# Kernel optimization log

Measured on AMD Instinct MI355X. Metric: run time of the kernel, lower is better.

Reference implementation:

```python
import jax, jax.numpy as jnp
import numpy as np

B, D, O, E, K = 8192, 2048, 2048, 8, 2


def setup_inputs() -> dict:
    key = jax.random.key(0)
    k1, k2, k3, k4 = jax.random.split(key, 4)
    x = jax.random.normal(k1, (B, D), dtype=jnp.float32)
    # router: Linear(D -> E)
    router_w = jax.random.normal(k2, (E, D), dtype=jnp.float32) * (1.0 / np.sqrt(D))
    router_b = jnp.zeros((E,), dtype=jnp.float32)
    # experts: [E, O, D] weight (xavier-uniform-like scale), [E, O] bias (zeros)
    lim = np.sqrt(6.0 / (D + O))
    expert_w = jax.random.uniform(k3, (E, O, D), dtype=jnp.float32, minval=-lim, maxval=lim)
    expert_b = jnp.zeros((E, O), dtype=jnp.float32)
    return {"x": x, "router_w": router_w, "router_b": router_b,
            "expert_w": expert_w, "expert_b": expert_b}


def reference(x, router_w, router_b, expert_w, expert_b):
    # router logits [B, E]
    logits = x @ router_w.T + router_b
    top_vals, top_idx = jax.lax.top_k(logits, K)          # [B, K]
    routing_weights = jax.nn.softmax(top_vals, axis=-1)   # softmax over top-k logits
    # dense per-(token, expert) combine weight [B, E]; zero for unselected experts
    onehot = jax.nn.one_hot(top_idx, E, dtype=x.dtype)    # [B, K, E]
    w_be = jnp.einsum('bk,bke->be', routing_weights, onehot)
    # per-expert linear, weighted combine (loop over small fixed E)
    out = jnp.zeros((x.shape[0], O), dtype=x.dtype)
    for e in range(E):
        out = out + w_be[:, e:e + 1] * (x @ expert_w[e].T + expert_b[e])
    return out
```

## Files before the change

### kernel.cpp

```cpp
#include <hip/hip_runtime.h>
#include <stdint.h>

#define NB 8192
#define ND 2048
#define NO 2048
#define NE 8
#define NT (ND / 32)

typedef __bf16 bf16x8 __attribute__((ext_vector_type(8)));
typedef float floatx4 __attribute__((ext_vector_type(4)));

__device__ __forceinline__ unsigned short f2bf(float f) {
    union { float f; uint32_t u; } v; v.f = f;
    uint32_t u = v.u;
    return (unsigned short)((u + 0x7FFFu + ((u >> 16) & 1u)) >> 16);
}

__global__ __launch_bounds__(256) void cvt_bf16_kernel(
        const float* __restrict__ b, unsigned short* __restrict__ ob, int n4) {
    int i = blockIdx.x * blockDim.x + threadIdx.x;
    int stride = gridDim.x * blockDim.x;
    for (; i < n4; i += stride) {
        float4 v = ((const float4*)b)[i];
        ushort4 o;
        o.x = f2bf(v.x); o.y = f2bf(v.y); o.z = f2bf(v.z); o.w = f2bf(v.w);
        ((ushort4*)ob)[i] = o;
    }
}

__global__ __launch_bounds__(256) void router_topk_kernel(const float* __restrict__ x,
        const float* __restrict__ rw, const float* __restrict__ rb,
        unsigned short* __restrict__ xbf,
        int* __restrict__ i0a, int* __restrict__ i1a,
        float* __restrict__ w0a, float* __restrict__ w1a) {
    const int wave = threadIdx.x >> 6;
    const int lane = threadIdx.x & 63;
    const int t = blockIdx.x * 4 + wave;
    const float4* xp = (const float4*)(x + (size_t)t * ND);
    const float4* rp = (const float4*)rw;
    ushort4* xo = (ushort4*)(xbf + (size_t)t * ND);
    float acc[NE];
#pragma unroll
    for (int e = 0; e < NE; e++) acc[e] = 0.f;
#pragma unroll
    for (int i = 0; i < ND / 256; i++) {
        int idx = i * 64 + lane;
        float4 xv = xp[idx];
        ushort4 o;
        o.x = f2bf(xv.x); o.y = f2bf(xv.y); o.z = f2bf(xv.z); o.w = f2bf(xv.w);
        xo[idx] = o;
#pragma unroll
        for (int e = 0; e < NE; e++) {
            float4 rv = rp[(size_t)e * (ND / 4) + idx];
            acc[e] += xv.x * rv.x + xv.y * rv.y + xv.z * rv.z + xv.w * rv.w;
        }
    }
#pragma unroll
    for (int e = 0; e < NE; e++) {
        float v = acc[e];
#pragma unroll
        for (int s = 32; s > 0; s >>= 1) v += __shfl_xor(v, s, 64);
        acc[e] = v;
    }
    if (lane == 0) {
        float lg[NE];
#pragma unroll
        for (int e = 0; e < NE; e++) lg[e] = acc[e] + rb[e];
        int i0 = 0; float v0 = lg[0];
#pragma unroll
        for (int e = 1; e < NE; e++) if (lg[e] > v0) { v0 = lg[e]; i0 = e; }
        int i1 = -1; float v1 = -3.4e38f;
#pragma unroll
        for (int e = 0; e < NE; e++) if (e != i0 && lg[e] > v1) { v1 = lg[e]; i1 = e; }
        float ex = expf(v1 - v0);
        float inv = 1.f / (1.f + ex);
        i0a[t] = i0; i1a[t] = i1;
        w0a[t] = inv; w1a[t] = ex * inv;
    }
}

__global__ __launch_bounds__(256) void compact_kernel(
        const int* __restrict__ i0a, const int* __restrict__ i1a,
        const float* __restrict__ w0a, const float* __restrict__ w1a,
        int* __restrict__ cnt, int* __restrict__ tok, float* __restrict__ wl) {
    const int lane = threadIdx.x & 63;
    const int gw = (blockIdx.x * 256 + threadIdx.x) >> 6;
    const int t = gw * 64 + lane;
#pragma unroll
    for (int which = 0; which < 2; which++) {
        int sel   = which ? i1a[t] : i0a[t];
        float w   = which ? w1a[t] : w0a[t];
        unsigned long long m[NE];
#pragma unroll
        for (int e = 0; e < NE; e++) m[e] = __ballot(sel == e);
        int slot = __popcll(m[sel] & ((1ull << lane) - 1ull));
        int base = 0;
        if (lane < NE) base = atomicAdd(&cnt[lane], (int)__popcll(m[lane]));
        base = __shfl(base, sel, 64);
        tok[sel * NB + base + slot] = t;
        wl[sel * NB + base + slot]  = w;
    }
}

#define GLL16(g, l) __builtin_amdgcn_global_load_lds( \
    (const __attribute__((address_space(1))) void*)(g), \
    (__attribute__((address_space(3))) void*)(l), 16, 0, 0)

__global__ __launch_bounds__(256, 3) void moe_gemm_kernel(
        const unsigned short* __restrict__ xbf, const unsigned short* __restrict__ wbf,
        const float* __restrict__ eb, const int* __restrict__ cntArr,
        const int* __restrict__ listTok, const float* __restrict__ listW,
        float* __restrict__ out) {
    __shared__ unsigned short sA[3][128 * 32];
    __shared__ unsigned short sB[3][128 * 32];
    __shared__ int sTok[128];
    __shared__ float sW[128];

    const int e = blockIdx.z, mt = blockIdx.y, nt = blockIdx.x;
    const int cnt = cntArr[e];
    if (mt * 128 >= cnt) return;
    const int tid = threadIdx.x;
    if (tid < 128) {
        int r = mt * 128 + tid;
        bool ok = r < cnt;
        sTok[tid] = ok ? listTok[e * NB + r] : 0;
        sW[tid]   = ok ? listW[e * NB + r] : 0.f;
    }
    __syncthreads();

    const char* gA[2]; const char* gB[2];
    int offAB[2];
#pragma unroll
    for (int r = 0; r < 2; r++) {
        int c = r * 256 + tid;
        int row = c >> 2, colb = (c & 3) * 16;
        gA[r] = (const char*)xbf + (size_t)sTok[row] * (ND * 2) + colb;
        gB[r] = (const char*)wbf + ((size_t)e * NO + (size_t)nt * 128 + row) * (ND * 2) + colb;
        offAB[r] = c * 16;
    }

    const int wave = tid >> 6, lane = tid & 63;
    const int wm = (wave >> 1) * 64, wn = (wave & 1) * 64;
    const int lr = lane & 15, lq = lane >> 4;
    int roA[4], roB[4];
#pragma unroll
    for (int i = 0; i < 4; i++) {
        roA[i] = (wm + i * 16 + lr) * 32 + lq * 8;
        roB[i] = (wn + i * 16 + lr) * 32 + lq * 8;
    }

    floatx4 acc[4][4];
#pragma unroll
    for (int mi = 0; mi < 4; mi++)
#pragma unroll
        for (int nj = 0; nj < 4; nj++) acc[mi][nj] = (floatx4){0.f, 0.f, 0.f, 0.f};

#pragma unroll
    for (int r = 0; r < 2; r++) {
        GLL16(gA[r], (char*)sA[0] + offAB[r]);
        GLL16(gB[r], (char*)sB[0] + offAB[r]);
        gA[r] += 64; gB[r] += 64;
    }
#pragma unroll
    for (int r = 0; r < 2; r++) {
        GLL16(gA[r], (char*)sA[1] + offAB[r]);
        GLL16(gB[r], (char*)sB[1] + offAB[r]);
        gA[r] += 64; gB[r] += 64;
    }

    int cur = 0;
#pragma unroll 1
    for (int t = 0; t < NT; t++) {
        int nxt = cur + 2; if (nxt >= 3) nxt -= 3;
        if (t + 2 < NT) {
#pragma unroll
            for (int r = 0; r < 2; r++) {
                GLL16(gA[r], (char*)sA[nxt] + offAB[r]);
                GLL16(gB[r], (char*)sB[nxt] + offAB[r]);
                gA[r] += 64; gB[r] += 64;
            }
            asm volatile("s_waitcnt vmcnt(8)" ::: "memory");
        } else if (t + 2 == NT) {
            asm volatile("s_waitcnt vmcnt(4)" ::: "memory");
        } else {
            asm volatile("s_waitcnt vmcnt(0)" ::: "memory");
        }
        __builtin_amdgcn_s_barrier();

        const unsigned short* sAc = sA[cur];
        const unsigned short* sBc = sB[cur];
        bf16x8 af[4], bfr[4];
#pragma unroll
        for (int mi = 0; mi < 4; mi++) af[mi] = *(const bf16x8*)&sAc[roA[mi]];
#pragma unroll
        for (int nj = 0; nj < 4; nj++) bfr[nj] = *(const bf16x8*)&sBc[roB[nj]];
#pragma unroll
        for (int mi = 0; mi < 4; mi++)
#pragma unroll
            for (int nj = 0; nj < 4; nj++)
                acc[mi][nj] = __builtin_amdgcn_mfma_f32_16x16x32_bf16(af[mi], bfr[nj], acc[mi][nj], 0, 0, 0);

        asm volatile("s_waitcnt lgkmcnt(0)" ::: "memory");
        __builtin_amdgcn_s_barrier();
        cur = cur + 1 == 3 ? 0 : cur + 1;
    }

#pragma unroll
    for (int nj = 0; nj < 4; nj++) {
        int gn = nt * 128 + wn + nj * 16 + lr;
        float bias = eb[(size_t)e * NO + gn];
#pragma unroll
        for (int mi = 0; mi < 4; mi++) {
#pragma unroll
            for (int r = 0; r < 4; r++) {
                int m = wm + mi * 16 + lq * 4 + r;
                if (mt * 128 + m < cnt) {
                    atomicAdd(out + (size_t)sTok[m] * NO + gn,
                              sW[m] * (acc[mi][nj][r] + bias));
                }
            }
        }
    }
}

extern "C" void kernel_launch(void* const* d_in, const int* in_sizes, int n_in,
                              void* d_out, int out_size, void* d_ws, size_t ws_size,
                              hipStream_t stream) {
    const float* x        = (const float*)d_in[0];
    const float* router_w = (const float*)d_in[1];
    const float* router_b = (const float*)d_in[2];
    const float* expert_w = (const float*)d_in[3];
    const float* expert_b = (const float*)d_in[4];
    float* out = (float*)d_out;
    char* ws = (char*)d_ws;

    unsigned short* xbf = (unsigned short*)ws;
    unsigned short* wbf = (unsigned short*)(ws + 33554432);
    size_t o = 100663296;
    int*   tokL = (int*)(ws + o);   o += NE * NB * 4;
    float* wL   = (float*)(ws + o); o += NE * NB * 4;
    int*   i0a  = (int*)(ws + o);   o += NB * 4;
    int*   i1a  = (int*)(ws + o);   o += NB * 4;
    float* w0a  = (float*)(ws + o); o += NB * 4;
    float* w1a  = (float*)(ws + o); o += NB * 4;
    int*   cnt  = (int*)(ws + o);   o += 128;

    hipMemsetAsync(cnt, 0, 128, stream);
    hipMemsetAsync(out, 0, (size_t)NB * NO * 4, stream);
    router_topk_kernel<<<NB / 4, 256, 0, stream>>>(x, router_w, router_b, xbf,
                                                   i0a, i1a, w0a, w1a);
    cvt_bf16_kernel<<<2048, 256, 0, stream>>>(expert_w, wbf, NE * NO * ND / 4);
    compact_kernel<<<NB / 64 / 4, 256, 0, stream>>>(i0a, i1a, w0a, w1a, cnt, tokL, wL);
    moe_gemm_kernel<<<dim3(NO / 128, NB / 128, NE), 256, 0, stream>>>(
        xbf, wbf, expert_b, cnt, tokL, wL, out);
}
```

Baseline: 591.4 us.

## Pre-gather routed token rows into packed per-expert bf16 buffer before GEMM

A new gather kernel converts x to bf16 and writes routed tokens contiguously per expert, so the MoE GEMM reads A rows sequentially instead of doing indirect per-row token loads. The output zeroing is folded into the weight-convert kernel and the counter reset moves into the router kernel, which removes two memsets. In exchange there is an extra pass that writes a 2*NB row buffer, and each GEMM block computes an expert prefix sum from the counts.

```diff
diff --git a/kernel.cpp b/kernel.cpp
--- a/kernel.cpp
+++ b/kernel.cpp
@@ -6,9 +6,12 @@
 #define NO 2048
 #define NE 8
 #define NT (ND / 32)
+#define NROWS (2 * NB)
+#define NROWS_PAD (NROWS + 128)
 
 typedef __bf16 bf16x8 __attribute__((ext_vector_type(8)));
 typedef float floatx4 __attribute__((ext_vector_type(4)));
+typedef unsigned short ushort8 __attribute__((ext_vector_type(8)));
 
 __device__ __forceinline__ unsigned short f2bf(float f) {
     union { float f; uint32_t u; } v; v.f = f;
@@ -16,29 +19,37 @@
     return (unsigned short)((u + 0x7FFFu + ((u >> 16) & 1u)) >> 16);
 }
 
-__global__ __launch_bounds__(256) void cvt_bf16_kernel(
-        const float* __restrict__ b, unsigned short* __restrict__ ob, int n4) {
+__global__ __launch_bounds__(256) void cvt_zero_kernel(
+        const float* __restrict__ w, unsigned short* __restrict__ ob,
+        float* __restrict__ out) {
+    const int n4W = NE * NO * ND / 4;
+    const int n4O = NB * NO / 4;
     int i = blockIdx.x * blockDim.x + threadIdx.x;
     int stride = gridDim.x * blockDim.x;
-    for (; i < n4; i += stride) {
-        float4 v = ((const float4*)b)[i];
-        ushort4 o;
-        o.x = f2bf(v.x); o.y = f2bf(v.y); o.z = f2bf(v.z); o.w = f2bf(v.w);
-        ((ushort4*)ob)[i] = o;
+    for (; i < n4W + n4O; i += stride) {
+        if (i < n4W) {
+            float4 v = ((const float4*)w)[i];
+            ushort4 o;
+            o.x = f2bf(v.x); o.y = f2bf(v.y); o.z = f2bf(v.z); o.w = f2bf(v.w);
+            ((ushort4*)ob)[i] = o;
+        } else {
+            float4 z = {0.f, 0.f, 0.f, 0.f};
+            ((float4*)out)[i - n4W] = z;
+        }
     }
 }
 
 __global__ __launch_bounds__(256) void router_topk_kernel(const float* __restrict__ x,
         const float* __restrict__ rw, const float* __restrict__ rb,
-        unsigned short* __restrict__ xbf,
         int* __restrict__ i0a, int* __restrict__ i1a,
-        float* __restrict__ w0a, float* __restrict__ w1a) {
+        float* __restrict__ w0a, float* __restrict__ w1a,
+        int* __restrict__ cnt) {
+    if (blockIdx.x == 0 && threadIdx.x < NE) cnt[threadIdx.x] = 0;
     const int wave = threadIdx.x >> 6;
     const int lane = threadIdx.x & 63;
     const int t = blockIdx.x * 4 + wave;
     const float4* xp = (const float4*)(x + (size_t)t * ND);
     const float4* rp = (const float4*)rw;
-    ushort4* xo = (ushort4*)(xbf + (size_t)t * ND);
     float acc[NE];
 #pragma unroll
     for (int e = 0; e < NE; e++) acc[e] = 0.f;
@@ -46,9 +57,6 @@
     for (int i = 0; i < ND / 256; i++) {
         int idx = i * 64 + lane;
         float4 xv = xp[idx];
-        ushort4 o;
-        o.x = f2bf(xv.x); o.y = f2bf(xv.y); o.z = f2bf(xv.z); o.w = f2bf(xv.w);
-        xo[idx] = o;
 #pragma unroll
         for (int e = 0; e < NE; e++) {
             float4 rv = rp[(size_t)e * (ND / 4) + idx];
@@ -102,12 +110,42 @@
     }
 }
 
+__global__ __launch_bounds__(256) void gather_kernel(
+        const float* __restrict__ x, const int* __restrict__ cnt,
+        const int* __restrict__ tokL, unsigned short* __restrict__ packed) {
+    int pre[NE + 1];
+    pre[0] = 0;
+#pragma unroll
+    for (int k = 0; k < NE; k++) pre[k + 1] = pre[k] + cnt[k];
+    const int CH = ND / 8;
+    int idx = blockIdx.x * blockDim.x + threadIdx.x;
+    const int stride = gridDim.x * blockDim.x;
+    const int tot = NROWS_PAD * CH;
+    for (; idx < tot; idx += stride) {
+        int p = idx >> 8;
+        int c = idx & (CH - 1);
+        int e = -1, r = 0;
+#pragma unroll
+        for (int k = 0; k < NE; k++)
+            if (p >= pre[k] && p < pre[k + 1]) { e = k; r = p - pre[k]; }
+        ushort8 o = (ushort8)0;
+        if (e >= 0) {
+            int tk = tokL[e * NB + r];
+            const float4* s = (const float4*)(x + (size_t)tk * ND + c * 8);
+            float4 a = s[0], b = s[1];
+            o[0] = f2bf(a.x); o[1] = f2bf(a.y); o[2] = f2bf(a.z); o[3] = f2bf(a.w);
+            o[4] = f2bf(b.x); o[5] = f2bf(b.y); o[6] = f2bf(b.z); o[7] = f2bf(b.w);
+        }
+        *(ushort8*)(packed + (size_t)p * ND + c * 8) = o;
+    }
+}
+
 #define GLL16(g, l) __builtin_amdgcn_global_load_lds( \
     (const __attribute__((address_space(1))) void*)(g), \
     (__attribute__((address_space(3))) void*)(l), 16, 0, 0)
 
 __global__ __launch_bounds__(256, 3) void moe_gemm_kernel(
-        const unsigned short* __restrict__ xbf, const unsigned short* __restrict__ wbf,
+        const unsigned short* __restrict__ packed, const unsigned short* __restrict__ wbf,
         const float* __restrict__ eb, const int* __restrict__ cntArr,
         const int* __restrict__ listTok, const float* __restrict__ listW,
         float* __restrict__ out) {
@@ -117,6 +155,8 @@
     __shared__ float sW[128];
 
     const int e = blockIdx.z, mt = blockIdx.y, nt = blockIdx.x;
+    int base = 0;
+    for (int i = 0; i < e; i++) base += cntArr[i];
     const int cnt = cntArr[e];
     if (mt * 128 >= cnt) return;
     const int tid = threadIdx.x;
@@ -134,7 +174,7 @@
     for (int r = 0; r < 2; r++) {
         int c = r * 256 + tid;
         int row = c >> 2, colb = (c & 3) * 16;
-        gA[r] = (const char*)xbf + (size_t)sTok[row] * (ND * 2) + colb;
+        gA[r] = (const char*)packed + (size_t)(base + mt * 128 + row) * (ND * 2) + colb;
         gB[r] = (const char*)wbf + ((size_t)e * NO + (size_t)nt * 128 + row) * (ND * 2) + colb;
         offAB[r] = c * 16;
     }
@@ -234,9 +274,9 @@
     float* out = (float*)d_out;
     char* ws = (char*)d_ws;
 
-    unsigned short* xbf = (unsigned short*)ws;
-    unsigned short* wbf = (unsigned short*)(ws + 33554432);
-    size_t o = 100663296;
+    unsigned short* wbf    = (unsigned short*)ws;
+    unsigned short* packed = (unsigned short*)(ws + 67108864);
+    size_t o = 67108864 + 67633152;
     int*   tokL = (int*)(ws + o);   o += NE * NB * 4;
     float* wL   = (float*)(ws + o); o += NE * NB * 4;
     int*   i0a  = (int*)(ws + o);   o += NB * 4;
@@ -245,12 +285,11 @@
     float* w1a  = (float*)(ws + o); o += NB * 4;
     int*   cnt  = (int*)(ws + o);   o += 128;
 
-    hipMemsetAsync(cnt, 0, 128, stream);
-    hipMemsetAsync(out, 0, (size_t)NB * NO * 4, stream);
-    router_topk_kernel<<<NB / 4, 256, 0, stream>>>(x, router_w, router_b, xbf,
-                                                   i0a, i1a, w0a, w1a);
-    cvt_bf16_kernel<<<2048, 256, 0, stream>>>(expert_w, wbf, NE * NO * ND / 4);
+    router_topk_kernel<<<NB / 4, 256, 0, stream>>>(x, router_w, router_b,
+                                                   i0a, i1a, w0a, w1a, cnt);
+    cvt_zero_kernel<<<2048, 256, 0, stream>>>(expert_w, wbf, out);
     compact_kernel<<<NB / 64 / 4, 256, 0, stream>>>(i0a, i1a, w0a, w1a, cnt, tokL, wL);
+    gather_kernel<<<2048, 256, 0, stream>>>(x, cnt, tokL, packed);
     moe_gemm_kernel<<<dim3(NO / 128, NB / 128, NE), 256, 0, stream>>>(
-        xbf, wbf, expert_b, cnt, tokL, wL, out);
-}
+        packed, wbf, expert_b, cnt, tokL, wL, out);
+}
```

Result: slower. 609.3 us (+3.0%).
